# Kernel tuning notes

Hardware: AMD Instinct MI355X
Metric: run time of the kernel (lower is better)

Reference implementation:

```python
import jax, jax.numpy as jnp
import numpy as np
from jax import lax

KSIZE = 3
SIGMA = 0.8
BLOCK = 8
DCT_THRESH = 2.5
DCT_CLIP = 10.0
DWT_LAM = 0.05


def _gaussian_kernel(dtype):
    coords = jnp.arange(KSIZE, dtype=dtype) - (KSIZE - 1) / 2.0
    grid = coords[None, :] ** 2 + coords[:, None] ** 2
    k = jnp.exp(-grid / (2.0 * SIGMA * SIGMA))
    return k / k.sum()


def gaussian_blur(x):
    # depthwise 3x3 gaussian with reflect padding, groups=C
    C = x.shape[1]
    k = _gaussian_kernel(x.dtype)
    kernel = jnp.broadcast_to(k[None, None], (C, 1, KSIZE, KSIZE))
    pad = KSIZE // 2
    xp = jnp.pad(x, ((0, 0), (0, 0), (pad, pad), (pad, pad)), mode='reflect')
    return lax.conv_general_dilated(
        xp, kernel, window_strides=(1, 1), padding='VALID',
        dimension_numbers=('NCHW', 'OIHW', 'NCHW'), feature_group_count=C)


def block_dct_normalize(x):
    # 8x8 block "DCT" implemented (as in the source) via fft2().real, then
    # soft shrink of small coeffs + clip, then ifft2().real reconstruction.
    B, C, H, W = x.shape
    Ph, Pw = H // BLOCK, W // BLOCK  # H, W chosen as multiples of 8 -> no pad
    blocks = x.reshape(B, C, Ph, BLOCK, Pw, BLOCK).transpose(0, 1, 2, 4, 3, 5)
    coeff = jnp.fft.fft2(blocks, norm='ortho').real
    ca = jnp.abs(coeff)
    coeff = jnp.where(ca < DCT_THRESH, coeff * (ca / (DCT_THRESH + 1e-8)), coeff)
    coeff = jnp.clip(coeff, -DCT_CLIP, DCT_CLIP)
    rec = jnp.fft.ifft2(coeff.astype(jnp.complex64), norm='ortho').real
    rec = rec.transpose(0, 1, 2, 4, 3, 5).reshape(B, C, H, W)
    return rec.astype(x.dtype)


def haar_dwt2(x):
    # orthonormal 2x2 Haar analysis; sign/order conventions cancel in the
    # soft-threshold + inverse pipeline (soft_threshold is odd in sign)
    B, C, H, W = x.shape
    r = x.reshape(B, C, H // 2, 2, W // 2, 2)
    a, b = r[:, :, :, 0, :, 0], r[:, :, :, 0, :, 1]
    c, d = r[:, :, :, 1, :, 0], r[:, :, :, 1, :, 1]
    LL = (a + b + c + d) * 0.5
    LH = (a + b - c - d) * 0.5
    HL = (a - b + c - d) * 0.5
    HH = (a - b - c + d) * 0.5
    return LL, LH, HL, HH


def haar_idwt2(LL, LH, HL, HH):
    B, C, Hh, Wh = LL.shape
    a = (LL + LH + HL + HH) * 0.5
    b = (LL + LH - HL - HH) * 0.5
    c = (LL - LH + HL - HH) * 0.5
    d = (LL - LH - HL + HH) * 0.5
    top = jnp.stack([a, b], axis=-1)  # (B,C,Hh,Wh,2)
    bot = jnp.stack([c, d], axis=-1)
    r = jnp.stack([top, bot], axis=3)  # (B,C,Hh,2,Wh,2)
    return r.reshape(B, C, 2 * Hh, 2 * Wh)


def soft_threshold(x, lam):
    return jnp.sign(x) * jnp.maximum(jnp.abs(x) - lam, 0.0)


def wavelet_refine(x):
    LL, LH, HL, HH = haar_dwt2(x)
    return haar_idwt2(LL, soft_threshold(LH, DWT_LAM),
                      soft_threshold(HL, DWT_LAM),
                      soft_threshold(HH, DWT_LAM))


def setup_inputs() -> dict:
    key = jax.random.key(0)
    I = jax.random.uniform(key, (32, 3, 512, 512), dtype=jnp.float32)
    return {"I": I}


def reference(I):
    I_g = gaussian_blur(I)
    I_d = block_dct_normalize(I_g)
    R_d = I_g - I_d
    I_d_wave = wavelet_refine(I_d)
    R_d_wave = wavelet_refine(R_d)
    # input_mode='concat', residual_type='R_d'
    return jnp.concatenate([I_d_wave, R_d_wave], axis=1)
```

## Files before the change

kernel.cpp:

```cpp
#include <hip/hip_runtime.h>

#define HW 512

__device__ __forceinline__ int reflect512(int v) {
    v = v < 0 ? -v : v;
    v = v > 511 ? 1022 - v : v;
    return v;
}

__device__ __forceinline__ float softt(float x) {
    return copysignf(fmaxf(fabsf(x) - 0.05f, 0.0f), x);
}

__device__ __forceinline__ void haar_quad(float a, float b, float c, float d,
                                          float& oa, float& ob, float& oc, float& od) {
    float LL = (a + b + c + d) * 0.5f;
    float LH = (a + b - c - d) * 0.5f;
    float HL = (a - b + c - d) * 0.5f;
    float HH = (a - b - c + d) * 0.5f;
    LH = softt(LH); HL = softt(HL); HH = softt(HH);
    oa = (LL + LH + HL + HH) * 0.5f;
    ob = (LL + LH - HL - HH) * 0.5f;
    oc = (LL - LH + HL - HH) * 0.5f;
    od = (LL - LH - HL + HH) * 0.5f;
}

#define RA 0.35355339059327373f
#define RB 0.25f

__device__ __forceinline__ void dft8_cos(const float* __restrict__ x, float* __restrict__ P) {
    float e0 = x[0] + x[4], d0 = x[0] - x[4];
    float e1 = x[2] + x[6];
    float o0 = x[1] + x[5], m0 = x[1] - x[5];
    float o1 = x[3] + x[7], m1 = x[3] - x[7];
    float see = e0 + e1, dee = e0 - e1, soo = o0 + o1;
    float dd = m0 - m1;
    P[0] = RA * (see + soo);
    P[4] = RA * (see - soo);
    float p2 = RA * dee;
    P[2] = p2; P[6] = p2;
    float t0 = RA * d0, t1 = RB * dd;
    P[1] = t0 + t1; P[7] = t0 + t1;
    P[3] = t0 - t1; P[5] = t0 - t1;
}

__device__ __forceinline__ void dft8_sin(const float* __restrict__ x, float* __restrict__ Q) {
    float d1 = x[2] - x[6];
    float o0 = x[1] + x[5], m0 = x[1] - x[5];
    float o1 = x[3] + x[7], m1 = x[3] - x[7];
    float qq = m0 + m1;
    Q[0] = 0.0f; Q[4] = 0.0f;
    float q2 = RA * (o0 - o1);
    Q[2] = q2; Q[6] = -q2;
    float t0 = RB * qq, t1 = RA * d1;
    Q[1] = t0 + t1; Q[7] = -(t0 + t1);
    Q[3] = t0 - t1; Q[5] = -(t0 - t1);
}

__launch_bounds__(256, 2)
__global__ void sas_fused(const float* __restrict__ in, float* __restrict__ out) {
    const int lane = threadIdx.x & 63;
    const int wv = threadIdx.x >> 6;
    const int p = blockIdx.y;
    const int by = blockIdx.x * 4 + wv;
    const float* __restrict__ inP = in + (size_t)p * (HW * HW);
    const int cx = lane * 8;

    float4 va[10], vb[10];
#pragma unroll
    for (int j = 0; j < 10; ++j) {
        int gy = reflect512(by * 8 - 1 + j);
        const float* r = inP + (size_t)gy * HW + cx;
        va[j] = *(const float4*)r;
        vb[j] = *(const float4*)(r + 4);
    }

    float x[10][10];
#pragma unroll
    for (int j = 0; j < 10; ++j) {
        float lft = __shfl_up(vb[j].w, 1);
        float rgt = __shfl_down(va[j].x, 1);
        if (lane == 0)  lft = va[j].y;
        if (lane == 63) rgt = vb[j].z;
        x[j][0] = lft;
        x[j][1] = va[j].x; x[j][2] = va[j].y; x[j][3] = va[j].z; x[j][4] = va[j].w;
        x[j][5] = vb[j].x; x[j][6] = vb[j].y; x[j][7] = vb[j].z; x[j][8] = vb[j].w;
        x[j][9] = rgt;
    }

    const float e = 0.45783336f;
    const float inv_s = 1.0f / ((1.0f + 2.0f * e) * (1.0f + 2.0f * e));
    float B[8][8];
#pragma unroll
    for (int j = 0; j < 8; ++j) {
        float v[10];
#pragma unroll
        for (int c = 0; c < 10; ++c)
            v[c] = e * (x[j][c] + x[j + 2][c]) + x[j + 1][c];
#pragma unroll
        for (int c = 0; c < 8; ++c)
            B[j][c] = (e * (v[c] + v[c + 2]) + v[c + 1]) * inv_s;
    }

    float P[8][8], Q[8][8];
#pragma unroll
    for (int m = 0; m < 8; ++m) { dft8_cos(B[m], P[m]); dft8_sin(B[m], Q[m]); }
#pragma unroll
    for (int v = 0; v < 8; ++v) {
        float pc[8], qc[8], tc[8], sc[8];
#pragma unroll
        for (int m = 0; m < 8; ++m) { pc[m] = P[m][v]; qc[m] = Q[m][v]; }
        dft8_cos(pc, tc);
        dft8_sin(qc, sc);
#pragma unroll
        for (int u = 0; u < 8; ++u) {
            float t = tc[u] - sc[u];
            float ca = fabsf(t);
            t = (ca < 2.5f) ? t * (ca * 0.4f) : t;
            t = fminf(fmaxf(t, -10.0f), 10.0f);
            P[u][v] = t;
        }
    }
#pragma unroll
    for (int m = 0; m < 8; ++m) {
        float tr[8];
#pragma unroll
        for (int n = 0; n < 8; ++n) tr[n] = P[m][n];
        dft8_cos(tr, P[m]);
        dft8_sin(tr, Q[m]);
    }
#pragma unroll
    for (int v = 0; v < 8; ++v) {
        float pc[8], qc[8], tc[8], sc[8];
#pragma unroll
        for (int m = 0; m < 8; ++m) { pc[m] = P[m][v]; qc[m] = Q[m][v]; }
        dft8_cos(pc, tc);
        dft8_sin(qc, sc);
#pragma unroll
        for (int u = 0; u < 8; ++u) P[u][v] = tc[u] - sc[u];
    }

    const int chId = (p / 3) * 6 + (p % 3);
    float* __restrict__ oI = out + ((size_t)chId << 18);
    float* __restrict__ oR = out + ((size_t)(chId + 3) << 18);
#pragma unroll
    for (int qy = 0; qy < 4; ++qy) {
        float ti[2][8], tr_[2][8];
#pragma unroll
        for (int qx = 0; qx < 4; ++qx) {
            float d00 = P[2*qy][2*qx],   d01 = P[2*qy][2*qx+1];
            float d10 = P[2*qy+1][2*qx], d11 = P[2*qy+1][2*qx+1];
            haar_quad(d00, d01, d10, d11,
                      ti[0][2*qx], ti[0][2*qx+1], ti[1][2*qx], ti[1][2*qx+1]);
            float r00 = B[2*qy][2*qx]   - d00, r01 = B[2*qy][2*qx+1]   - d01;
            float r10 = B[2*qy+1][2*qx] - d10, r11 = B[2*qy+1][2*qx+1] - d11;
            haar_quad(r00, r01, r10, r11,
                      tr_[0][2*qx], tr_[0][2*qx+1], tr_[1][2*qx], tr_[1][2*qx+1]);
        }
        size_t base = (size_t)(by * 8 + 2 * qy) * HW + cx;
        *(float4*)&oI[base]          = make_float4(ti[0][0], ti[0][1], ti[0][2], ti[0][3]);
        *(float4*)&oI[base + 4]      = make_float4(ti[0][4], ti[0][5], ti[0][6], ti[0][7]);
        *(float4*)&oI[base + HW]     = make_float4(ti[1][0], ti[1][1], ti[1][2], ti[1][3]);
        *(float4*)&oI[base + HW + 4] = make_float4(ti[1][4], ti[1][5], ti[1][6], ti[1][7]);
        *(float4*)&oR[base]          = make_float4(tr_[0][0], tr_[0][1], tr_[0][2], tr_[0][3]);
        *(float4*)&oR[base + 4]      = make_float4(tr_[0][4], tr_[0][5], tr_[0][6], tr_[0][7]);
        *(float4*)&oR[base + HW]     = make_float4(tr_[1][0], tr_[1][1], tr_[1][2], tr_[1][3]);
        *(float4*)&oR[base + HW + 4] = make_float4(tr_[1][4], tr_[1][5], tr_[1][6], tr_[1][7]);
    }
}

extern "C" void kernel_launch(void* const* d_in, const int* in_sizes, int n_in,
                              void* d_out, int out_size, void* d_ws, size_t ws_size,
                              hipStream_t stream) {
    const float* I = (const float*)d_in[0];
    float* out = (float*)d_out;
    dim3 grid(16, 96);
    sas_fused<<<grid, dim3(256), 0, stream>>>(I, out);
}
```

Measured before the change: 279.1 us.

## Exploit DFT real-part symmetries, stream blur rows, and use nontemporal stores

```diff
diff --git a/kernel.cpp b/kernel.cpp
--- a/kernel.cpp
+++ b/kernel.cpp
@@ -1,6 +1,10 @@
 #include <hip/hip_runtime.h>
 
 #define HW 512
+#define RA 0.35355339059327373f
+#define RB 0.25f
+
+typedef float fvec4 __attribute__((ext_vector_type(4)));
 
 __device__ __forceinline__ int reflect512(int v) {
     v = v < 0 ? -v : v;
@@ -8,56 +12,80 @@
     return v;
 }
 
-__device__ __forceinline__ float softt(float x) {
-    return copysignf(fmaxf(fabsf(x) - 0.05f, 0.0f), x);
+__device__ __forceinline__ float softt2(float x) {
+    return copysignf(fmaxf(fabsf(x) - 0.1f, 0.0f), x);
+}
+
+__device__ __forceinline__ float nlin(float t) {
+    float ca = fabsf(t);
+    t = (ca < 2.5f) ? t * (ca * 0.4f) : t;
+    return fminf(fmaxf(t, -10.0f), 10.0f);
 }
 
 __device__ __forceinline__ void haar_quad(float a, float b, float c, float d,
                                           float& oa, float& ob, float& oc, float& od) {
-    float LL = (a + b + c + d) * 0.5f;
-    float LH = (a + b - c - d) * 0.5f;
-    float HL = (a - b + c - d) * 0.5f;
-    float HH = (a - b - c + d) * 0.5f;
-    LH = softt(LH); HL = softt(HL); HH = softt(HH);
-    oa = (LL + LH + HL + HH) * 0.5f;
-    ob = (LL + LH - HL - HH) * 0.5f;
-    oc = (LL - LH + HL - HH) * 0.5f;
-    od = (LL - LH - HL + HH) * 0.5f;
-}
-
-#define RA 0.35355339059327373f
-#define RB 0.25f
-
-__device__ __forceinline__ void dft8_cos(const float* __restrict__ x, float* __restrict__ P) {
+    float s1 = a + b, s2 = c + d, d1 = a - b, d2 = c - d;
+    float LL = s1 + s2, LH = s1 - s2, HL = d1 + d2, HH = d1 - d2;
+    LH = softt2(LH); HL = softt2(HL); HH = softt2(HH);
+    float u1 = LL + LH, u2 = HL + HH, w1 = LL - LH, w2 = HL - HH;
+    oa = (u1 + u2) * 0.25f; ob = (u1 - u2) * 0.25f;
+    oc = (w1 + w2) * 0.25f; od = (w1 - w2) * 0.25f;
+}
+
+__device__ __forceinline__ void cos5(const float* __restrict__ x, float* __restrict__ t) {
     float e0 = x[0] + x[4], d0 = x[0] - x[4];
     float e1 = x[2] + x[6];
     float o0 = x[1] + x[5], m0 = x[1] - x[5];
     float o1 = x[3] + x[7], m1 = x[3] - x[7];
-    float see = e0 + e1, dee = e0 - e1, soo = o0 + o1;
-    float dd = m0 - m1;
-    P[0] = RA * (see + soo);
-    P[4] = RA * (see - soo);
-    float p2 = RA * dee;
-    P[2] = p2; P[6] = p2;
-    float t0 = RA * d0, t1 = RB * dd;
-    P[1] = t0 + t1; P[7] = t0 + t1;
-    P[3] = t0 - t1; P[5] = t0 - t1;
-}
-
-__device__ __forceinline__ void dft8_sin(const float* __restrict__ x, float* __restrict__ Q) {
+    float see = e0 + e1, dee = e0 - e1, soo = o0 + o1, dd = m0 - m1;
+    t[0] = RA * (see + soo);
+    t[4] = RA * (see - soo);
+    t[2] = RA * dee;
+    float a = RA * d0, b = RB * dd;
+    t[1] = a + b;
+    t[3] = a - b;
+}
+
+__device__ __forceinline__ void sin3(const float* __restrict__ x, float* __restrict__ s) {
     float d1 = x[2] - x[6];
-    float o0 = x[1] + x[5], m0 = x[1] - x[5];
+    float m0 = x[1] - x[5];
+    float o0 = x[1] + x[5];
     float o1 = x[3] + x[7], m1 = x[3] - x[7];
     float qq = m0 + m1;
-    Q[0] = 0.0f; Q[4] = 0.0f;
-    float q2 = RA * (o0 - o1);
-    Q[2] = q2; Q[6] = -q2;
-    float t0 = RB * qq, t1 = RA * d1;
-    Q[1] = t0 + t1; Q[7] = -(t0 + t1);
-    Q[3] = t0 - t1; Q[5] = -(t0 - t1);
-}
-
-__launch_bounds__(256, 2)
+    float a = RB * qq, b = RA * d1;
+    s[0] = a + b;
+    s[1] = RA * (o0 - o1);
+    s[2] = a - b;
+}
+
+__device__ __forceinline__ void cos5_sym(const float* __restrict__ x, float* __restrict__ t) {
+    float e0 = x[0] + x[4], d0 = x[0] - x[4];
+    float tx2 = 2.0f * x[2];
+    float see = e0 + tx2, dee = e0 - tx2;
+    float soo = 2.0f * (x[1] + x[3]);
+    float m0 = x[1] - x[3];
+    t[0] = RA * (see + soo);
+    t[4] = RA * (see - soo);
+    t[2] = RA * dee;
+    float a = RA * d0, b = 0.5f * m0;
+    t[1] = a + b;
+    t[3] = a - b;
+}
+
+__device__ __forceinline__ void sin3_asym(const float* __restrict__ y, float* __restrict__ s) {
+    float a = 0.5f * (y[0] + y[2]);
+    float b = (2.0f * RA) * y[1];
+    s[0] = a + b;
+    s[1] = (2.0f * RA) * (y[0] - y[2]);
+    s[2] = a - b;
+}
+
+__device__ __forceinline__ void nt_store4(float* p, float a, float b, float c, float d) {
+    fvec4 v = {a, b, c, d};
+    __builtin_nontemporal_store(v, (fvec4*)p);
+}
+
+__launch_bounds__(256, 3)
 __global__ void sas_fused(const float* __restrict__ in, float* __restrict__ out) {
     const int lane = threadIdx.x & 63;
     const int wv = threadIdx.x >> 6;
@@ -66,78 +94,140 @@
     const float* __restrict__ inP = in + (size_t)p * (HW * HW);
     const int cx = lane * 8;
 
-    float4 va[10], vb[10];
+    const float e = 0.45783336f;
+    const float inv_s = 1.0f / ((1.0f + 2.0f * e) * (1.0f + 2.0f * e));
+
+    float B[8][8];
+    float h[3][8];
 #pragma unroll
     for (int j = 0; j < 10; ++j) {
         int gy = reflect512(by * 8 - 1 + j);
         const float* r = inP + (size_t)gy * HW + cx;
-        va[j] = *(const float4*)r;
-        vb[j] = *(const float4*)(r + 4);
-    }
-
-    float x[10][10];
-#pragma unroll
-    for (int j = 0; j < 10; ++j) {
-        float lft = __shfl_up(vb[j].w, 1);
-        float rgt = __shfl_down(va[j].x, 1);
-        if (lane == 0)  lft = va[j].y;
-        if (lane == 63) rgt = vb[j].z;
-        x[j][0] = lft;
-        x[j][1] = va[j].x; x[j][2] = va[j].y; x[j][3] = va[j].z; x[j][4] = va[j].w;
-        x[j][5] = vb[j].x; x[j][6] = vb[j].y; x[j][7] = vb[j].z; x[j][8] = vb[j].w;
-        x[j][9] = rgt;
-    }
-
-    const float e = 0.45783336f;
-    const float inv_s = 1.0f / ((1.0f + 2.0f * e) * (1.0f + 2.0f * e));
-    float B[8][8];
-#pragma unroll
-    for (int j = 0; j < 8; ++j) {
-        float v[10];
-#pragma unroll
-        for (int c = 0; c < 10; ++c)
-            v[c] = e * (x[j][c] + x[j + 2][c]) + x[j + 1][c];
+        float4 va = *(const float4*)r;
+        float4 vb = *(const float4*)(r + 4);
+        float lft = __shfl_up(vb.w, 1);
+        float rgt = __shfl_down(va.x, 1);
+        if (lane == 0)  lft = va.y;
+        if (lane == 63) rgt = vb.z;
+        float xr[10] = {lft, va.x, va.y, va.z, va.w, vb.x, vb.y, vb.z, vb.w, rgt};
+        float* hc = h[j % 3];
 #pragma unroll
         for (int c = 0; c < 8; ++c)
-            B[j][c] = (e * (v[c] + v[c + 2]) + v[c + 1]) * inv_s;
-    }
-
-    float P[8][8], Q[8][8];
-#pragma unroll
-    for (int m = 0; m < 8; ++m) { dft8_cos(B[m], P[m]); dft8_sin(B[m], Q[m]); }
-#pragma unroll
-    for (int v = 0; v < 8; ++v) {
-        float pc[8], qc[8], tc[8], sc[8];
-#pragma unroll
-        for (int m = 0; m < 8; ++m) { pc[m] = P[m][v]; qc[m] = Q[m][v]; }
-        dft8_cos(pc, tc);
-        dft8_sin(qc, sc);
-#pragma unroll
-        for (int u = 0; u < 8; ++u) {
-            float t = tc[u] - sc[u];
-            float ca = fabsf(t);
-            t = (ca < 2.5f) ? t * (ca * 0.4f) : t;
-            t = fminf(fmaxf(t, -10.0f), 10.0f);
-            P[u][v] = t;
-        }
-    }
+            hc[c] = e * (xr[c] + xr[c + 2]) + xr[c + 1];
+        if (j >= 2) {
+            const float* h0 = h[(j - 2) % 3];
+            const float* h1 = h[(j - 1) % 3];
+#pragma unroll
+            for (int c = 0; c < 8; ++c)
+                B[j - 2][c] = (e * (h0[c] + hc[c]) + h1[c]) * inv_s;
+        }
+    }
+
+    float cpT[5][8], spT[3][8];
 #pragma unroll
     for (int m = 0; m < 8; ++m) {
-        float tr[8];
-#pragma unroll
-        for (int n = 0; n < 8; ++n) tr[n] = P[m][n];
-        dft8_cos(tr, P[m]);
-        dft8_sin(tr, Q[m]);
-    }
-#pragma unroll
-    for (int v = 0; v < 8; ++v) {
-        float pc[8], qc[8], tc[8], sc[8];
-#pragma unroll
-        for (int m = 0; m < 8; ++m) { pc[m] = P[m][v]; qc[m] = Q[m][v]; }
-        dft8_cos(pc, tc);
-        dft8_sin(qc, sc);
-#pragma unroll
-        for (int u = 0; u < 8; ++u) P[u][v] = tc[u] - sc[u];
+        float t[5], s[3];
+        cos5(B[m], t);
+        sin3(B[m], s);
+#pragma unroll
+        for (int v = 0; v < 5; ++v) cpT[v][m] = t[v];
+#pragma unroll
+        for (int v = 0; v < 3; ++v) spT[v][m] = s[v];
+    }
+
+    float Tc0[5], Tc4[5];
+    cos5(cpT[0], Tc0);
+    cos5(cpT[4], Tc4);
+    float Tt[3], Tb[3], TA[3][3], TB[3][3];
+#pragma unroll
+    for (int vi = 0; vi < 3; ++vi) {
+        float t[5], s[3];
+        cos5(cpT[vi + 1], t);
+        sin3(spT[vi], s);
+        Tt[vi] = t[0];
+        Tb[vi] = t[4];
+#pragma unroll
+        for (int ui = 0; ui < 3; ++ui) {
+            TA[vi][ui] = t[ui + 1] - s[ui];
+            TB[vi][ui] = t[ui + 1] + s[ui];
+        }
+    }
+
+#pragma unroll
+    for (int i = 0; i < 5; ++i) { Tc0[i] = nlin(Tc0[i]); Tc4[i] = nlin(Tc4[i]); }
+#pragma unroll
+    for (int vi = 0; vi < 3; ++vi) {
+        Tt[vi] = nlin(Tt[vi]);
+        Tb[vi] = nlin(Tb[vi]);
+#pragma unroll
+        for (int ui = 0; ui < 3; ++ui) {
+            TA[vi][ui] = nlin(TA[vi][ui]);
+            TB[vi][ui] = nlin(TB[vi][ui]);
+        }
+    }
+
+    float p2[5][5], q2[3][3];
+    {
+        float x0[5] = {Tc0[0], Tt[0], Tt[1], Tt[2], Tc4[0]};
+        cos5_sym(x0, p2[0]);
+        float x4[5] = {Tc0[4], Tb[0], Tb[1], Tb[2], Tc4[4]};
+        cos5_sym(x4, p2[4]);
+    }
+#pragma unroll
+    for (int u = 1; u <= 3; ++u) {
+        float r8[8] = {Tc0[u], TA[0][u - 1], TA[1][u - 1], TA[2][u - 1], Tc4[u],
+                       TB[2][u - 1], TB[1][u - 1], TB[0][u - 1]};
+        cos5(r8, p2[u]);
+        sin3(r8, q2[u - 1]);
+    }
+
+    float Rc0[5], Rc4[5];
+    {
+        float c0[5] = {p2[0][0], p2[1][0], p2[2][0], p2[3][0], p2[4][0]};
+        cos5_sym(c0, Rc0);
+        float c4[5] = {p2[0][4], p2[1][4], p2[2][4], p2[3][4], p2[4][4]};
+        cos5_sym(c4, Rc4);
+    }
+    float r0v[3], r4v[3], RAm[3][3], RBm[3][3];
+#pragma unroll
+    for (int vi = 0; vi < 3; ++vi) {
+        int v = vi + 1;
+        float cs[5] = {p2[0][v], p2[1][v], p2[2][v], p2[3][v], p2[4][v]};
+        float t[5];
+        cos5_sym(cs, t);
+        float y[3] = {q2[0][vi], q2[1][vi], q2[2][vi]};
+        float s[3];
+        sin3_asym(y, s);
+        r0v[vi] = t[0];
+        r4v[vi] = t[4];
+#pragma unroll
+        for (int ui = 0; ui < 3; ++ui) {
+            RAm[vi][ui] = t[ui + 1] - s[ui];
+            RBm[vi][ui] = t[ui + 1] + s[ui];
+        }
+    }
+
+    float rec[8][8];
+#pragma unroll
+    for (int u = 0; u < 8; ++u) {
+        int us = (u <= 4) ? u : 8 - u;
+        rec[u][0] = Rc0[us];
+        rec[u][4] = Rc4[us];
+    }
+#pragma unroll
+    for (int v = 1; v < 8; ++v) {
+        if (v == 4) continue;
+        int vs = (v <= 4) ? v : 8 - v;
+        bool vf = v > 4;
+        rec[0][v] = r0v[vs - 1];
+        rec[4][v] = r4v[vs - 1];
+#pragma unroll
+        for (int u = 1; u < 8; ++u) {
+            if (u == 4) continue;
+            int us = (u <= 4) ? u : 8 - u;
+            bool uf = u > 4;
+            rec[u][v] = (vf != uf) ? RBm[vs - 1][us - 1] : RAm[vs - 1][us - 1];
+        }
     }
 
     const int chId = (p / 3) * 6 + (p % 3);
@@ -148,24 +238,24 @@
         float ti[2][8], tr_[2][8];
 #pragma unroll
         for (int qx = 0; qx < 4; ++qx) {
-            float d00 = P[2*qy][2*qx],   d01 = P[2*qy][2*qx+1];
-            float d10 = P[2*qy+1][2*qx], d11 = P[2*qy+1][2*qx+1];
+            float d00 = rec[2 * qy][2 * qx],     d01 = rec[2 * qy][2 * qx + 1];
+            float d10 = rec[2 * qy + 1][2 * qx], d11 = rec[2 * qy + 1][2 * qx + 1];
             haar_quad(d00, d01, d10, d11,
-                      ti[0][2*qx], ti[0][2*qx+1], ti[1][2*qx], ti[1][2*qx+1]);
-            float r00 = B[2*qy][2*qx]   - d00, r01 = B[2*qy][2*qx+1]   - d01;
-            float r10 = B[2*qy+1][2*qx] - d10, r11 = B[2*qy+1][2*qx+1] - d11;
+                      ti[0][2 * qx], ti[0][2 * qx + 1], ti[1][2 * qx], ti[1][2 * qx + 1]);
+            float r00 = B[2 * qy][2 * qx]     - d00, r01 = B[2 * qy][2 * qx + 1]     - d01;
+            float r10 = B[2 * qy + 1][2 * qx] - d10, r11 = B[2 * qy + 1][2 * qx + 1] - d11;
             haar_quad(r00, r01, r10, r11,
-                      tr_[0][2*qx], tr_[0][2*qx+1], tr_[1][2*qx], tr_[1][2*qx+1]);
+                      tr_[0][2 * qx], tr_[0][2 * qx + 1], tr_[1][2 * qx], tr_[1][2 * qx + 1]);
         }
         size_t base = (size_t)(by * 8 + 2 * qy) * HW + cx;
-        *(float4*)&oI[base]          = make_float4(ti[0][0], ti[0][1], ti[0][2], ti[0][3]);
-        *(float4*)&oI[base + 4]      = make_float4(ti[0][4], ti[0][5], ti[0][6], ti[0][7]);
-        *(float4*)&oI[base + HW]     = make_float4(ti[1][0], ti[1][1], ti[1][2], ti[1][3]);
-        *(float4*)&oI[base + HW + 4] = make_float4(ti[1][4], ti[1][5], ti[1][6], ti[1][7]);
-        *(float4*)&oR[base]          = make_float4(tr_[0][0], tr_[0][1], tr_[0][2], tr_[0][3]);
-        *(float4*)&oR[base + 4]      = make_float4(tr_[0][4], tr_[0][5], tr_[0][6], tr_[0][7]);
-        *(float4*)&oR[base + HW]     = make_float4(tr_[1][0], tr_[1][1], tr_[1][2], tr_[1][3]);
-        *(float4*)&oR[base + HW + 4] = make_float4(tr_[1][4], tr_[1][5], tr_[1][6], tr_[1][7]);
+        nt_store4(&oI[base],          ti[0][0], ti[0][1], ti[0][2], ti[0][3]);
+        nt_store4(&oI[base + 4],      ti[0][4], ti[0][5], ti[0][6], ti[0][7]);
+        nt_store4(&oI[base + HW],     ti[1][0], ti[1][1], ti[1][2], ti[1][3]);
+        nt_store4(&oI[base + HW + 4], ti[1][4], ti[1][5], ti[1][6], ti[1][7]);
+        nt_store4(&oR[base],          tr_[0][0], tr_[0][1], tr_[0][2], tr_[0][3]);
+        nt_store4(&oR[base + 4],      tr_[0][4], tr_[0][5], tr_[0][6], tr_[0][7]);
+        nt_store4(&oR[base + HW],     tr_[1][0], tr_[1][1], tr_[1][2], tr_[1][3]);
+        nt_store4(&oR[base + HW + 4], tr_[1][4], tr_[1][5], tr_[1][6], tr_[1][7]);
     }
 }
 
```

Result: slower. 325.5 us (+16.6%).
